# Optimization experiments

Hardware: AMD Instinct MI355X
Metric: run time of the kernel (lower is better)

The kernel has to match this reference:

```python
import jax, jax.numpy as jnp
import numpy as np

NUM_HEADS = 8
KEY_DIM = 16
BLOCK = 8
HALO = 3
KV_K = BLOCK + 2 * HALO          # kv_kernel = 14
EMB = NUM_HEADS * KEY_DIM        # 128


def setup_inputs() -> dict:
    key = jax.random.key(0)
    ks = jax.random.split(key, 6)
    B, H, W, C = 8, 80, 80, 128
    std = KEY_DIM ** -0.5
    return {
        "inputs": jax.random.normal(ks[0], (B, H, W, C), jnp.float32),
        "query_dense": jax.random.normal(ks[1], (C, EMB), jnp.float32) * 0.05,
        "kv_dense": jax.random.normal(ks[2], (C, 2 * EMB), jnp.float32) * 0.05,
        "out_dense": jax.random.normal(ks[3], (EMB, C), jnp.float32) * 0.05,
        "pos_emb_w": jax.random.normal(ks[4], (KEY_DIM, 2 * KV_K - 1), jnp.float32) * std,
        "pos_emb_h": jax.random.normal(ks[5], (KEY_DIM, 2 * KV_K - 1), jnp.float32) * std,
    }


def rel_to_abs(rel_pos):
    # [b, heads, hh, ww, 2*pos_dim-1] -> [b, heads, hh, ww, pos_dim]
    b, heads, hh, ww, dim = rel_pos.shape
    pos_dim = (dim + 1) // 2
    gap = pos_dim - ww if ww > 1 else 2
    flat = rel_pos.reshape(b, heads, hh, ww * dim)
    flat = flat[:, :, :, ww - 1:-1] if ww > 1 else flat[:, :, :, 1:]
    out = flat.reshape(b, heads, hh, ww, 2 * (pos_dim - 1))
    return out[..., gap:pos_dim + gap]


def relative_logits(pos_q, pe_w, pe_h):
    # pos_q: [b, n, qb, qb, key_dim]
    rl_w = rel_to_abs(jnp.einsum('bnxyd,dk->bnxyk', pos_q, pe_w))                       # [b,n,qb,qb,KV_K]
    qh = pos_q.transpose(0, 1, 3, 2, 4)
    rl_h = rel_to_abs(jnp.einsum('bnxyd,dk->bnxyk', qh, pe_h)).transpose(0, 1, 3, 2, 4)  # [b,n,qb,qb,KV_K]
    return rl_w[..., None, :] + rl_h[..., :, None]                                       # [b,n,qb,qb,KV_K,KV_K]


def reference(inputs, query_dense, kv_dense, out_dense, pos_emb_w, pos_emb_h):
    B, H, W, C = inputs.shape
    scale = 1.0 / jnp.sqrt(jnp.asarray(KEY_DIM, inputs.dtype))
    query = jnp.einsum('bhwc,cd->bhwd', inputs, query_dense) * scale
    hq, wq = H // BLOCK, W // BLOCK
    q = query.reshape(B, hq, BLOCK, wq, BLOCK, NUM_HEADS, KEY_DIM).transpose(0, 5, 1, 3, 2, 4, 6)
    attn_q = q.reshape(B, NUM_HEADS, hq, wq, BLOCK * BLOCK, KEY_DIM)
    pos_q = q.reshape(B, NUM_HEADS * hq * wq, BLOCK, BLOCK, KEY_DIM)

    kv = jnp.einsum('bhwc,cd->bhwd', inputs, kv_dense)
    kvp = jnp.pad(kv, ((0, 0), (HALO, HALO), (HALO, HALO), (0, 0)))
    # overlapping halo windows: stride BLOCK, window KV_K (matches tf.image.extract_patches)
    ridx = jnp.arange(hq)[:, None] * BLOCK + jnp.arange(KV_K)[None, :]
    cidx = jnp.arange(wq)[:, None] * BLOCK + jnp.arange(KV_K)[None, :]
    patches = kvp[:, ridx][:, :, :, cidx]                 # [B,hq,KV,wq,KV,2*EMB]
    patches = patches.transpose(0, 1, 3, 2, 4, 5)         # [B,hq,wq,KV,KV,2*EMB]
    kv_inp = patches.reshape(B, hq, wq, KV_K, KV_K, NUM_HEADS, 2 * KEY_DIM)
    kv_inp = kv_inp.transpose(0, 5, 1, 2, 3, 4, 6).reshape(B, NUM_HEADS, hq, wq, KV_K * KV_K, 2 * KEY_DIM)
    k, v = kv_inp[..., :KEY_DIM], kv_inp[..., KEY_DIM:]

    scores = jnp.einsum('bnhwqd,bnhwkd->bnhwqk', attn_q, k)   # [B,heads,hq,wq,64,196]
    pos = relative_logits(pos_q, pos_emb_w, pos_emb_h)
    scores = scores + pos.reshape(scores.shape)
    attn = jax.nn.softmax(scores, axis=-1)
    out = jnp.einsum('bnhwqk,bnhwkd->bnhwqd', attn, v)
    out = out.reshape(B, NUM_HEADS, hq, wq, BLOCK, BLOCK, KEY_DIM)
    out = out.transpose(0, 2, 4, 3, 5, 1, 6).reshape(B, H, W, EMB)
    return jnp.einsum('bhwe,eo->bhwo', out, out_dense)
```

## Files before the change

### kernel.cpp

```cpp
#include <hip/hip_runtime.h>
#include <cstddef>

namespace {
constexpr int BATCH = 8;
constexpr int HDIM  = 80;
constexpr int WDIM  = 80;
constexpr int CDIM  = 128;
constexpr int NH    = 8;
constexpr int KD    = 16;
constexpr int BLK   = 8;
constexpr int HALO  = 3;
constexpr int KVK   = 14;
constexpr int EMB   = 128;
constexpr int HQ    = 10;
constexpr int WQ    = 10;
constexpr int MROWS = BATCH * HDIM * WDIM;
constexpr int QKV_N = 384;

constexpr int KPAD  = 24;
constexpr int QPAD  = 24;
constexpr int VPAD  = 228;
constexpr int MPAD  = 21;
constexpr int PEPAD = 20;
constexpr int APAD  = 136;
}

typedef _Float16 f16;
typedef f16   f16x2 __attribute__((ext_vector_type(2)));
typedef f16   f16x4 __attribute__((ext_vector_type(4)));
typedef f16   f16x8 __attribute__((ext_vector_type(8)));
typedef float f32x4 __attribute__((ext_vector_type(4)));

__global__ __launch_bounds__(256) void convert_weights(
    const float* __restrict__ qd, const float* __restrict__ kvd,
    const float* __restrict__ od, f16* __restrict__ BTqkv, f16* __restrict__ BTo)
{
  const float QSC = 0.25f * 1.4426950408889634f;
  int tid = blockIdx.x * 256 + threadIdx.x;
  if (tid < 384 * 128) {
    int n = tid >> 7, c = tid & 127;
    float v = (n < 128) ? qd[c * 128 + n] * QSC : kvd[c * 256 + (n - 128)];
    BTqkv[tid] = (f16)v;
  } else {
    int j = tid - 384 * 128;
    int o = j >> 7, e = j & 127;
    BTo[j] = (f16)od[e * 128 + o];
  }
}

__global__ __launch_bounds__(256) void gemm_qkv_mfma(
    const float* __restrict__ A, const f16* __restrict__ BT,
    f16* __restrict__ C)
{
  __shared__ __align__(16) f16 a_lds[128 * APAD];
  __shared__ __align__(16) f16 b_lds[128 * APAD];

  const int bid = blockIdx.x;
  const int xcd = bid & 7;
  const int idx = bid >> 3;
  const int m0 = (xcd * 50 + idx / 3) * 128;
  const int n0 = (idx % 3) * 128;
  const int t  = threadIdx.x;

  #pragma unroll
  for (int it = 0; it < 16; ++it) {
    int item = t + it * 256;
    int row = item >> 5, c4 = item & 31;
    float4 v = *reinterpret_cast<const float4*>(
        A + (size_t)(m0 + row) * CDIM + c4 * 4);
    f16x4 h = {(f16)v.x, (f16)v.y, (f16)v.z, (f16)v.w};
    *reinterpret_cast<f16x4*>(&a_lds[row * APAD + c4 * 4]) = h;
  }
  #pragma unroll
  for (int it = 0; it < 8; ++it) {
    int item = t + it * 256;
    int row = item >> 4, c8 = item & 15;
    *reinterpret_cast<f16x8*>(&b_lds[row * APAD + c8 * 8]) =
        *reinterpret_cast<const f16x8*>(BT + (size_t)(n0 + row) * CDIM + c8 * 8);
  }
  __syncthreads();

  const int lane = t & 63, wv = t >> 6;
  const int g = lane >> 4, qi = lane & 15;

  f32x4 acc[2][8];
  #pragma unroll
  for (int mt = 0; mt < 2; ++mt)
    #pragma unroll
    for (int nt = 0; nt < 8; ++nt) acc[mt][nt] = {0.f, 0.f, 0.f, 0.f};

  #pragma unroll
  for (int ks = 0; ks < 8; ++ks) {
    f16x4 a0 = *reinterpret_cast<const f16x4*>(
        &a_lds[(wv * 32 + qi) * APAD + ks * 16 + g * 4]);
    f16x4 a1 = *reinterpret_cast<const f16x4*>(
        &a_lds[(wv * 32 + 16 + qi) * APAD + ks * 16 + g * 4]);
    #pragma unroll
    for (int nt = 0; nt < 8; ++nt) {
      f16x4 bf = *reinterpret_cast<const f16x4*>(
          &b_lds[(nt * 16 + qi) * APAD + ks * 16 + g * 4]);
      acc[0][nt] = __builtin_amdgcn_mfma_f32_16x16x16f16(bf, a0, acc[0][nt], 0, 0, 0);
      acc[1][nt] = __builtin_amdgcn_mfma_f32_16x16x16f16(bf, a1, acc[1][nt], 0, 0, 0);
    }
  }

  #pragma unroll
  for (int mt = 0; mt < 2; ++mt) {
    int m = m0 + wv * 32 + mt * 16 + qi;
    #pragma unroll
    for (int nt = 0; nt < 8; ++nt) {
      f16x4 h = {(f16)acc[mt][nt][0], (f16)acc[mt][nt][1],
                 (f16)acc[mt][nt][2], (f16)acc[mt][nt][3]};
      *reinterpret_cast<f16x4*>(&C[(size_t)m * QKV_N + n0 + nt * 16 + g * 4]) = h;
    }
  }
}

__global__ __launch_bounds__(256, 5) void halo_attn_mfma(
    const f16* __restrict__ qkv, const float* __restrict__ pew,
    const float* __restrict__ peh, f16* __restrict__ O)
{
  __shared__ __align__(16) f16 k_lds[224 * KPAD];
  __shared__ __align__(16) f16 vt_lds[16 * VPAD];
  __shared__ __align__(16) f16 q_lds[64 * QPAD];
  __shared__ __align__(16) f16 pet_lds[2 * 32 * PEPAD];
  __shared__ __align__(16) f16 m_lds[2 * 64 * MPAD];

  const int bid  = blockIdx.x;
  const int n    = bid & 7;
  const int tile = bid >> 3;
  const int tw   = tile % WQ;
  const int th   = (tile / WQ) % HQ;
  const int b    = tile / (WQ * HQ);
  const int t    = threadIdx.x;

  #pragma unroll
  for (int it = 0; it < 4; ++it) {
    int item = t + it * 256;
    if (item < 896) {
      int slot = item >> 2, part = item & 3;
      int kh = slot >> 4, kw = slot & 15;
      int hh = th * BLK - HALO + kh;
      int ww = tw * BLK - HALO + kw;
      f16x8 v = {};
      if ((unsigned)hh < (unsigned)HDIM && (unsigned)ww < (unsigned)WDIM) {
        size_t row = ((size_t)(b * HDIM + hh)) * WDIM + ww;
        v = *reinterpret_cast<const f16x8*>(
            &qkv[row * QKV_N + 128 + n * 32 + part * 8]);
      }
      if (part < 2) {
        *reinterpret_cast<f16x8*>(&k_lds[slot * KPAD + part * 8]) = v;
      } else {
        int d0 = (part - 2) * 8;
        #pragma unroll
        for (int j = 0; j < 8; ++j)
          vt_lds[(d0 + j) * VPAD + slot] = v[j];
      }
    }
  }
  if (t < 128) {
    int q = t >> 1, h = t & 1;
    size_t qrow = ((size_t)(b * HDIM + th * BLK + (q >> 3))) * WDIM + tw * BLK + (q & 7);
    *reinterpret_cast<f16x8*>(&q_lds[q * QPAD + h * 8]) =
        *reinterpret_cast<const f16x8*>(&qkv[qrow * QKV_N + n * KD + h * 8]);
  }
  #pragma unroll
  for (int it = 0; it < 4; ++it) {
    int item = t + it * 256;
    int which = item >> 9, d = (item >> 5) & 15, col = item & 31;
    if (col < 27) {
      float v = (which ? peh : pew)[d * 27 + col];
      pet_lds[(which * 32 + col) * PEPAD + d] = (f16)v;
    }
  }
  __syncthreads();

  const int lane = t & 63;
  const int wv   = t >> 6;
  const int g    = lane >> 4;
  const int qi   = lane & 15;
  const int q0   = wv * 16;
  const int q    = q0 + qi;
  const int x    = q >> 3, y = q & 7;

  const f32x4 z4 = {0.f, 0.f, 0.f, 0.f};
  f16x4 qf = *reinterpret_cast<const f16x4*>(&q_lds[q * QPAD + g * 4]);

  #pragma unroll
  for (int which = 0; which < 2; ++which) {
    #pragma unroll
    for (int ct = 0; ct < 2; ++ct) {
      f16x4 pf = *reinterpret_cast<const f16x4*>(
          &pet_lds[(which * 32 + ct * 16 + qi) * PEPAD + g * 4]);
      f32x4 mc = __builtin_amdgcn_mfma_f32_16x16x16f16(qf, pf, z4, 0, 0, 0);
      int col = ct * 16 + qi;
      if (col >= 6 && col <= 26) {
        #pragma unroll
        for (int r = 0; r < 4; ++r)
          m_lds[(which * 64 + q0 + g * 4 + r) * MPAD + (col - 6)] = (f16)mc[r];
      }
    }
  }

  f32x4 s[14];
  #pragma unroll
  for (int tt = 0; tt < 14; ++tt) {
    f16x4 kf = *reinterpret_cast<const f16x4*>(&k_lds[(tt * 16 + qi) * KPAD + g * 4]);
    s[tt] = __builtin_amdgcn_mfma_f32_16x16x16f16(kf, qf, z4, 0, 0, 0);
  }

  float rlw[4];
  #pragma unroll
  for (int r = 0; r < 4; ++r)
    rlw[r] = (g * 4 + r < KVK) ? (float)m_lds[q * MPAD + (g * 4 + r - y + 7)] : 0.f;
  const bool mk = (g == 3);

  float mx = -1e30f;
  #pragma unroll
  for (int tt = 0; tt < 14; ++tt) {
    float rh = (float)m_lds[(64 + q) * MPAD + (tt - x + 7)];
    s[tt][0] += rlw[0] + rh;
    s[tt][1] += rlw[1] + rh;
    s[tt][2] = mk ? -1e30f : s[tt][2] + rlw[2] + rh;
    s[tt][3] = mk ? -1e30f : s[tt][3] + rlw[3] + rh;
    mx = fmaxf(mx, fmaxf(fmaxf(s[tt][0], s[tt][1]), fmaxf(s[tt][2], s[tt][3])));
  }
  mx = fmaxf(mx, __shfl_xor(mx, 16));
  mx = fmaxf(mx, __shfl_xor(mx, 32));

  float ls = 0.f;
  f16x4 pf[14];
  #pragma unroll
  for (int tt = 0; tt < 14; ++tt) {
    float p0 = __builtin_amdgcn_exp2f(s[tt][0] - mx);
    float p1 = __builtin_amdgcn_exp2f(s[tt][1] - mx);
    float p2 = __builtin_amdgcn_exp2f(s[tt][2] - mx);
    float p3 = __builtin_amdgcn_exp2f(s[tt][3] - mx);
    ls += (p0 + p1) + (p2 + p3);
    f16x2 lo = __builtin_bit_cast(f16x2, __builtin_amdgcn_cvt_pkrtz(p0, p1));
    f16x2 hi = __builtin_bit_cast(f16x2, __builtin_amdgcn_cvt_pkrtz(p2, p3));
    pf[tt][0] = lo[0]; pf[tt][1] = lo[1];
    pf[tt][2] = hi[0]; pf[tt][3] = hi[1];
  }
  ls += __shfl_xor(ls, 16);
  ls += __shfl_xor(ls, 32);

  f32x4 acc = z4;
  #pragma unroll
  for (int tt = 0; tt < 14; ++tt) {
    f16x4 vf = *reinterpret_cast<const f16x4*>(&vt_lds[qi * VPAD + tt * 16 + g * 4]);
    acc = __builtin_amdgcn_mfma_f32_16x16x16f16(vf, pf[tt], acc, 0, 0, 0);
  }

  const float inv = __builtin_amdgcn_rcpf(ls);
  size_t orow = ((size_t)(b * HDIM + th * BLK + x)) * WDIM + tw * BLK + y;
  f16x4 o = {(f16)(acc[0] * inv), (f16)(acc[1] * inv),
             (f16)(acc[2] * inv), (f16)(acc[3] * inv)};
  *reinterpret_cast<f16x4*>(&O[orow * EMB + n * KD + g * 4]) = o;
}

__global__ __launch_bounds__(256) void gemm_out_mfma(
    const f16* __restrict__ A, const f16* __restrict__ BT,
    float* __restrict__ C)
{
  __shared__ __align__(16) f16 a_lds[64 * APAD];
  __shared__ __align__(16) f16 b_lds[128 * APAD];

  const int m0 = blockIdx.x * 64;
  const int t  = threadIdx.x;

  #pragma unroll
  for (int it = 0; it < 4; ++it) {
    int item = t + it * 256;
    int row = item >> 4, c8 = item & 15;
    *reinterpret_cast<f16x8*>(&a_lds[row * APAD + c8 * 8]) =
        *reinterpret_cast<const f16x8*>(A + (size_t)(m0 + row) * EMB + c8 * 8);
  }
  #pragma unroll
  for (int it = 0; it < 8; ++it) {
    int item = t + it * 256;
    int row = item >> 4, c8 = item & 15;
    *reinterpret_cast<f16x8*>(&b_lds[row * APAD + c8 * 8]) =
        *reinterpret_cast<const f16x8*>(BT + (size_t)row * EMB + c8 * 8);
  }
  __syncthreads();

  const int lane = t & 63, wv = t >> 6;
  const int g = lane >> 4, qi = lane & 15;

  f32x4 acc[8];
  #pragma unroll
  for (int nt = 0; nt < 8; ++nt) acc[nt] = {0.f, 0.f, 0.f, 0.f};

  #pragma unroll
  for (int ks = 0; ks < 8; ++ks) {
    f16x4 a = *reinterpret_cast<const f16x4*>(
        &a_lds[(wv * 16 + qi) * APAD + ks * 16 + g * 4]);
    #pragma unroll
    for (int nt = 0; nt < 8; ++nt) {
      f16x4 bf = *reinterpret_cast<const f16x4*>(
          &b_lds[(nt * 16 + qi) * APAD + ks * 16 + g * 4]);
      acc[nt] = __builtin_amdgcn_mfma_f32_16x16x16f16(bf, a, acc[nt], 0, 0, 0);
    }
  }

  const int m = m0 + wv * 16 + qi;
  #pragma unroll
  for (int nt = 0; nt < 8; ++nt) {
    f32x4 v = acc[nt];
    *reinterpret_cast<float4*>(&C[(size_t)m * CDIM + nt * 16 + g * 4]) =
        *reinterpret_cast<float4*>(&v);
  }
}

extern "C" void kernel_launch(void* const* d_in, const int* in_sizes, int n_in,
                              void* d_out, int out_size, void* d_ws, size_t ws_size,
                              hipStream_t stream)
{
  const float* inputs = (const float*)d_in[0];
  const float* qd     = (const float*)d_in[1];
  const float* kvd    = (const float*)d_in[2];
  const float* od     = (const float*)d_in[3];
  const float* pew    = (const float*)d_in[4];
  const float* peh    = (const float*)d_in[5];

  char* ws = (char*)d_ws;
  f16* qkv   = (f16*)ws;
  f16* O     = (f16*)(ws + (size_t)MROWS * QKV_N * 2);
  f16* BTqkv = (f16*)(ws + (size_t)MROWS * QKV_N * 2 + (size_t)MROWS * EMB * 2);
  f16* BTo   = BTqkv + 384 * 128;
  float* out = (float*)d_out;

  convert_weights<<<dim3((384 * 128 + 128 * 128) / 256), 256, 0, stream>>>(
      qd, kvd, od, BTqkv, BTo);
  gemm_qkv_mfma<<<dim3(1200), 256, 0, stream>>>(inputs, BTqkv, qkv);
  halo_attn_mfma<<<dim3(BATCH * HQ * WQ * NH), 256, 0, stream>>>(qkv, pew, peh, O);
  gemm_out_mfma<<<dim3(MROWS / 64), 256, 0, stream>>>(O, BTo, out);
}
```

Measured before the change: 82.78 us.

## Precompute fp16 positional tables, load Q directly, fold rel-logits into MFMA accumulator

Positional embedding tables are converted to transposed fp16 once, in the weight-conversion kernel, instead of in every attention block. Q fragments are loaded straight from global memory into registers rather than staged through LDS. The relative-logit bias is passed as the MFMA accumulator input, which removes a separate add pass, and the block index is remapped across XCDs. Occupancy drops from 5 to 4 blocks, and the m_lds write and read now rely on wave-local data in front of the barrier, which risks an LDS ordering hazard.

```diff
diff --git a/kernel.cpp b/kernel.cpp
--- a/kernel.cpp
+++ b/kernel.cpp
@@ -18,9 +18,8 @@
 constexpr int QKV_N = 384;
 
 constexpr int KPAD  = 24;
-constexpr int QPAD  = 24;
 constexpr int VPAD  = 228;
-constexpr int MPAD  = 21;
+constexpr int MPAD  = 34;
 constexpr int PEPAD = 20;
 constexpr int APAD  = 136;
 }
@@ -33,7 +32,9 @@
 
 __global__ __launch_bounds__(256) void convert_weights(
     const float* __restrict__ qd, const float* __restrict__ kvd,
-    const float* __restrict__ od, f16* __restrict__ BTqkv, f16* __restrict__ BTo)
+    const float* __restrict__ od, const float* __restrict__ pew,
+    const float* __restrict__ peh,
+    f16* __restrict__ BTqkv, f16* __restrict__ BTo, f16* __restrict__ peT)
 {
   const float QSC = 0.25f * 1.4426950408889634f;
   int tid = blockIdx.x * 256 + threadIdx.x;
@@ -41,10 +42,19 @@
     int n = tid >> 7, c = tid & 127;
     float v = (n < 128) ? qd[c * 128 + n] * QSC : kvd[c * 256 + (n - 128)];
     BTqkv[tid] = (f16)v;
-  } else {
+  } else if (tid < 384 * 128 + 128 * 128) {
     int j = tid - 384 * 128;
     int o = j >> 7, e = j & 127;
     BTo[j] = (f16)od[e * 128 + o];
+  } else {
+    int j = tid - (384 * 128 + 128 * 128);
+    int which = j / 640;
+    int rem   = j - which * 640;
+    int col   = rem / PEPAD;
+    int d     = rem - col * PEPAD;
+    float v = 0.f;
+    if (col < 27 && d < 16) v = (which ? peh : pew)[d * 27 + col];
+    peT[j] = (f16)v;
   }
 }
 
@@ -116,23 +126,33 @@
   }
 }
 
-__global__ __launch_bounds__(256, 5) void halo_attn_mfma(
-    const f16* __restrict__ qkv, const float* __restrict__ pew,
-    const float* __restrict__ peh, f16* __restrict__ O)
+__global__ __launch_bounds__(256, 4) void halo_attn_mfma(
+    const f16* __restrict__ qkv, const f16* __restrict__ peT,
+    f16* __restrict__ O)
 {
   __shared__ __align__(16) f16 k_lds[224 * KPAD];
   __shared__ __align__(16) f16 vt_lds[16 * VPAD];
-  __shared__ __align__(16) f16 q_lds[64 * QPAD];
-  __shared__ __align__(16) f16 pet_lds[2 * 32 * PEPAD];
   __shared__ __align__(16) f16 m_lds[2 * 64 * MPAD];
 
-  const int bid  = blockIdx.x;
+  const int d0w  = blockIdx.x;
+  const int bid  = (d0w & 7) * 800 + (d0w >> 3);
   const int n    = bid & 7;
   const int tile = bid >> 3;
   const int tw   = tile % WQ;
   const int th   = (tile / WQ) % HQ;
   const int b    = tile / (WQ * HQ);
   const int t    = threadIdx.x;
+
+  const int lane = t & 63;
+  const int wv   = t >> 6;
+  const int g    = lane >> 4;
+  const int qi   = lane & 15;
+  const int q0   = wv * 16;
+  const int q    = q0 + qi;
+  const int x    = q >> 3, y = q & 7;
+
+  const size_t qrow = ((size_t)(b * HDIM + th * BLK + x)) * WDIM + tw * BLK + y;
+  f16x4 qf = *reinterpret_cast<const f16x4*>(&qkv[qrow * QKV_N + n * KD + g * 4]);
 
   #pragma unroll
   for (int it = 0; it < 4; ++it) {
@@ -151,80 +171,53 @@
       if (part < 2) {
         *reinterpret_cast<f16x8*>(&k_lds[slot * KPAD + part * 8]) = v;
       } else {
-        int d0 = (part - 2) * 8;
+        int dd = (part - 2) * 8;
         #pragma unroll
         for (int j = 0; j < 8; ++j)
-          vt_lds[(d0 + j) * VPAD + slot] = v[j];
+          vt_lds[(dd + j) * VPAD + slot] = v[j];
       }
     }
   }
-  if (t < 128) {
-    int q = t >> 1, h = t & 1;
-    size_t qrow = ((size_t)(b * HDIM + th * BLK + (q >> 3))) * WDIM + tw * BLK + (q & 7);
-    *reinterpret_cast<f16x8*>(&q_lds[q * QPAD + h * 8]) =
-        *reinterpret_cast<const f16x8*>(&qkv[qrow * QKV_N + n * KD + h * 8]);
-  }
-  #pragma unroll
-  for (int it = 0; it < 4; ++it) {
-    int item = t + it * 256;
-    int which = item >> 9, d = (item >> 5) & 15, col = item & 31;
-    if (col < 27) {
-      float v = (which ? peh : pew)[d * 27 + col];
-      pet_lds[(which * 32 + col) * PEPAD + d] = (f16)v;
-    }
-  }
-  __syncthreads();
-
-  const int lane = t & 63;
-  const int wv   = t >> 6;
-  const int g    = lane >> 4;
-  const int qi   = lane & 15;
-  const int q0   = wv * 16;
-  const int q    = q0 + qi;
-  const int x    = q >> 3, y = q & 7;
 
   const f32x4 z4 = {0.f, 0.f, 0.f, 0.f};
-  f16x4 qf = *reinterpret_cast<const f16x4*>(&q_lds[q * QPAD + g * 4]);
 
   #pragma unroll
   for (int which = 0; which < 2; ++which) {
     #pragma unroll
     for (int ct = 0; ct < 2; ++ct) {
       f16x4 pf = *reinterpret_cast<const f16x4*>(
-          &pet_lds[(which * 32 + ct * 16 + qi) * PEPAD + g * 4]);
+          &peT[(which * 32 + ct * 16 + qi) * PEPAD + g * 4]);
       f32x4 mc = __builtin_amdgcn_mfma_f32_16x16x16f16(qf, pf, z4, 0, 0, 0);
-      int col = ct * 16 + qi;
-      if (col >= 6 && col <= 26) {
-        #pragma unroll
-        for (int r = 0; r < 4; ++r)
-          m_lds[(which * 64 + q0 + g * 4 + r) * MPAD + (col - 6)] = (f16)mc[r];
-      }
-    }
-  }
+      int colb = ct * 16 + qi;
+      #pragma unroll
+      for (int r = 0; r < 4; ++r)
+        m_lds[(which * 64 + q0 + g * 4 + r) * MPAD + colb] = (f16)mc[r];
+    }
+  }
+
+  float rlw[4];
+  #pragma unroll
+  for (int r = 0; r < 4; ++r)
+    rlw[r] = (float)m_lds[q * MPAD + (g * 4 + r) - y + 13];
+  if (g == 3) { rlw[2] = -1e30f; rlw[3] = -1e30f; }
+
+  __syncthreads();
 
   f32x4 s[14];
   #pragma unroll
   for (int tt = 0; tt < 14; ++tt) {
+    float rh = (float)m_lds[(64 + q) * MPAD + tt - x + 13];
+    f32x4 c;
+    c[0] = rlw[0] + rh; c[1] = rlw[1] + rh;
+    c[2] = rlw[2] + rh; c[3] = rlw[3] + rh;
     f16x4 kf = *reinterpret_cast<const f16x4*>(&k_lds[(tt * 16 + qi) * KPAD + g * 4]);
-    s[tt] = __builtin_amdgcn_mfma_f32_16x16x16f16(kf, qf, z4, 0, 0, 0);
-  }
-
-  float rlw[4];
-  #pragma unroll
-  for (int r = 0; r < 4; ++r)
-    rlw[r] = (g * 4 + r < KVK) ? (float)m_lds[q * MPAD + (g * 4 + r - y + 7)] : 0.f;
-  const bool mk = (g == 3);
+    s[tt] = __builtin_amdgcn_mfma_f32_16x16x16f16(kf, qf, c, 0, 0, 0);
+  }
 
   float mx = -1e30f;
   #pragma unroll
-  for (int tt = 0; tt < 14; ++tt) {
-    float rh = (float)m_lds[(64 + q) * MPAD + (tt - x + 7)];
-    s[tt][0] += rlw[0] + rh;
-    s[tt][1] += rlw[1] + rh;
-    s[tt][2] = mk ? -1e30f : s[tt][2] + rlw[2] + rh;
-    s[tt][3] = mk ? -1e30f : s[tt][3] + rlw[3] + rh;
-    mx = fmaxf(mx, fmaxf(fmaxf(s[tt][0], s[tt][1]), fmaxf(s[tt][2], s[tt][3])));
-  }
+  for (int tt = 0; tt < 14; ++tt)
+    mx = fmaxf(fmaxf(fmaxf(s[tt][0], s[tt][1]), fmaxf(s[tt][2], s[tt][3])), mx);
   mx = fmaxf(mx, __shfl_xor(mx, 16));
   mx = fmaxf(mx, __shfl_xor(mx, 32));
 
@@ -253,10 +246,9 @@
   }
 
   const float inv = __builtin_amdgcn_rcpf(ls);
-  size_t orow = ((size_t)(b * HDIM + th * BLK + x)) * WDIM + tw * BLK + y;
   f16x4 o = {(f16)(acc[0] * inv), (f16)(acc[1] * inv),
              (f16)(acc[2] * inv), (f16)(acc[3] * inv)};
-  *reinterpret_cast<f16x4*>(&O[orow * EMB + n * KD + g * 4]) = o;
+  *reinterpret_cast<f16x4*>(&O[qrow * EMB + n * KD + g * 4]) = o;
 }
 
 __global__ __launch_bounds__(256) void gemm_out_mfma(
@@ -329,11 +321,12 @@
   f16* O     = (f16*)(ws + (size_t)MROWS * QKV_N * 2);
   f16* BTqkv = (f16*)(ws + (size_t)MROWS * QKV_N * 2 + (size_t)MROWS * EMB * 2);
   f16* BTo   = BTqkv + 384 * 128;
+  f16* peT   = BTo + 128 * 128;
   float* out = (float*)d_out;
 
-  convert_weights<<<dim3((384 * 128 + 128 * 128) / 256), 256, 0, stream>>>(
-      qd, kvd, od, BTqkv, BTo);
+  convert_weights<<<dim3(261), 256, 0, stream>>>(qd, kvd, od, pew, peh,
+                                                 BTqkv, BTo, peT);
   gemm_qkv_mfma<<<dim3(1200), 256, 0, stream>>>(inputs, BTqkv, qkv);
-  halo_attn_mfma<<<dim3(BATCH * HQ * WQ * NH), 256, 0, stream>>>(qkv, pew, peh, O);
+  halo_attn_mfma<<<dim3(BATCH * HQ * WQ * NH), 256, 0, stream>>>(qkv, peT, O);
   gemm_out_mfma<<<dim3(MROWS / 64), 256, 0, stream>>>(O, BTo, out);
 }
```

Result: faster. 77.68 us (-6.2%).
